# Kernel tuning notes

Measured on AMD Instinct MI355X. Metric: run time of the kernel, lower is better.

Reference implementation:

```python
import jax, jax.numpy as jnp
import numpy as np

N = [80000, 70000, 50000]   # entities per type (flattened over the ragged batch)
F = [64, 128, 48]           # feature width per entity type
D = 512                     # d_model
B = 64                      # number of episodes in the ragged batch
EPS_IN = 1e-4               # InputNorm eps
EPS_LN = 1e-5               # LayerNorm eps
CLIP = 5.0                  # InputNorm cliprange


def setup_inputs() -> dict:
    key = jax.random.key(0)
    ks = jax.random.split(key, 3 * 7 + 2)
    inp = {}
    for i, (n, f) in enumerate(zip(N, F)):
        base = 7 * i
        inp[f"ent{i}"] = jax.random.normal(ks[base], (n, f), dtype=jnp.float32)
        inp[f"mean{i}"] = 0.1 * jax.random.normal(ks[base + 1], (f,), dtype=jnp.float32)
        inp[f"var{i}"] = jax.random.uniform(ks[base + 2], (f,), minval=0.5, maxval=1.5, dtype=jnp.float32)
        inp[f"W{i}"] = jax.random.normal(ks[base + 3], (f, D), dtype=jnp.float32) / np.sqrt(f)
        inp[f"b{i}"] = jnp.zeros((D,), dtype=jnp.float32)
        inp[f"gamma{i}"] = jnp.ones((D,), dtype=jnp.float32)
        inp[f"beta{i}"] = jnp.zeros((D,), dtype=jnp.float32)
    total = sum(N)
    # index_map: permutation reassembling per-type blocks into ragged episode order
    inp["index_map"] = jax.random.permutation(ks[-2], total).astype(jnp.int64)
    inp["batch_index"] = jnp.sort(jax.random.randint(ks[-1], (total,), 0, B)).astype(jnp.int64)
    return inp


def _embed(x, mean, var, W, b, gamma, beta):
    # InputNorm: normalize with running stats, clip outliers
    h = jnp.clip((x - mean) * jax.lax.rsqrt(var + EPS_IN), -CLIP, CLIP)
    # Linear + ReLU
    h = jnp.maximum(h @ W + b, 0.0)
    # LayerNorm
    mu = h.mean(-1, keepdims=True)
    v = ((h - mu) ** 2).mean(-1, keepdims=True)
    return gamma * (h - mu) * jax.lax.rsqrt(v + EPS_LN) + beta


def reference(ent0, mean0, var0, W0, b0, gamma0, beta0,
              ent1, mean1, var1, W1, b1, gamma1, beta1,
              ent2, mean2, var2, W2, b2, gamma2, beta2,
              index_map, batch_index):
    embeds = [
        _embed(ent0, mean0, var0, W0, b0, gamma0, beta0),
        _embed(ent1, mean1, var1, W1, b1, gamma1, beta1),
        _embed(ent2, mean2, var2, W2, b2, gamma2, beta2),
    ]
    x = jnp.concatenate(embeds, axis=0)                      # [sum(N), D]
    entity_type = jnp.concatenate(
        [jnp.full((n, 1), float(i), dtype=jnp.float32) for i, n in enumerate(N)], axis=0
    )
    # ragged reorder: gather-based reassembly into episode-major order
    x = x[index_map]
    entity_types = entity_type[index_map]
    tbatch_index = batch_index[index_map]
    return x, tbatch_index, entity_types
```

## Files before the change

kernel.cpp:

```cpp
#include <hip/hip_runtime.h>

#define DMODEL 512
#define EPS_IN 1e-4f
#define EPS_LN 1e-5f
#define CLIPV  5.0f

typedef float f32x4 __attribute__((ext_vector_type(4)));
typedef short s16x8 __attribute__((ext_vector_type(8)));

__device__ __forceinline__ unsigned short f2bf(float f) {
    union { float f; unsigned u; } v; v.f = f;
    unsigned r = v.u + 0x7fffu + ((v.u >> 16) & 1u);
    return (unsigned short)(r >> 16);
}

struct TypeParams {
    const float* x;
    const float* ss;
    const unsigned short* Wt;
    const float* b; const float* gamma; const float* beta;
    int n;
    int offset;
    int nb;
};

__global__ __launch_bounds__(256) void setup_all(
    const int* __restrict__ index_map, const int* __restrict__ batch_index,
    int* __restrict__ inv, float* __restrict__ out_t, float* __restrict__ out_e,
    int total, int n0, int n01, int nbA,
    const float* __restrict__ W0, const float* __restrict__ W1, const float* __restrict__ W2,
    unsigned short* __restrict__ Wt0, unsigned short* __restrict__ Wt1, unsigned short* __restrict__ Wt2,
    const float* __restrict__ mean0, const float* __restrict__ var0,
    const float* __restrict__ mean1, const float* __restrict__ var1,
    const float* __restrict__ mean2, const float* __restrict__ var2,
    float* __restrict__ ss0, float* __restrict__ ss1, float* __restrict__ ss2)
{
    const int nbB = (DMODEL * 256) / 256;
    if (blockIdx.x < (unsigned)nbA) {
        const int j = blockIdx.x * 256 + threadIdx.x;
        if (j >= total) return;
        const int r = index_map[j];
        inv[r] = j;
        out_t[j] = (float)batch_index[r];
        out_e[j] = (r < n0) ? 0.0f : ((r < n01) ? 1.0f : 2.0f);
    } else if (blockIdx.x < (unsigned)(nbA + nbB)) {
        int idx = (blockIdx.x - nbA) * 256 + threadIdx.x;
        const float* W; unsigned short* Wt; int K, Kp;
        if (idx < DMODEL * 64)              { W = W0; Wt = Wt0; K = 64;  Kp = 64; }
        else if (idx < DMODEL * (64 + 128)) { idx -= DMODEL * 64;  W = W1; Wt = Wt1; K = 128; Kp = 128; }
        else                                { idx -= DMODEL * 192; W = W2; Wt = Wt2; K = 48;  Kp = 64; }
        const int nn = idx / Kp, k = idx - nn * Kp;
        const float w = (k < K) ? W[(size_t)k * DMODEL + nn] : 0.0f;
        Wt[idx] = f2bf(w);
    } else {
        const int c = threadIdx.x;
        if (c < 64)  { const float s = rsqrtf(var0[c] + EPS_IN); ss0[c] = s; ss0[64 + c]  = -mean0[c] * s; }
        if (c < 128) { const float s = rsqrtf(var1[c] + EPS_IN); ss1[c] = s; ss1[128 + c] = -mean1[c] * s; }
        if (c < 48)  { const float s = rsqrtf(var2[c] + EPS_IN); ss2[c] = s; ss2[48 + c]  = -mean2[c] * s; }
    }
}

template<int F, int KP>
__device__ __forceinline__ void embed_body(
    const TypeParams& p, int bid, const int* __restrict__ inv,
    float* __restrict__ out, char* lds)
{
    const int tid  = threadIdx.x;
    const int lane = tid & 63;
    const int wn   = tid >> 6;
    const int l15  = lane & 15;
    const int g    = lane >> 4;
    const int row0 = bid * 32;
    const int n    = p.n;
    constexpr int SEG = KP / 8;
    constexpr int NKS = KP / 32;

    float2* red = reinterpret_cast<float2*>(lds + NKS * 2048);

    if (tid < 32 * SEG) {
        const int r = tid & 31;
        const int s = tid >> 5;
        const int gr = row0 + r;
        const int c = s * 8;
        s16x8 pk;
#pragma unroll
        for (int jj = 0; jj < 8; ++jj) pk[jj] = 0;
        if (gr < n && c < F) {
            const float4 x0 = *(const float4*)(p.x + (size_t)gr * F + c);
            const float4 x1 = *(const float4*)(p.x + (size_t)gr * F + c + 4);
            const float4 sc0 = *(const float4*)(p.ss + c);
            const float4 sc1 = *(const float4*)(p.ss + c + 4);
            const float4 sh0 = *(const float4*)(p.ss + F + c);
            const float4 sh1 = *(const float4*)(p.ss + F + c + 4);
            float t[8];
            t[0] = fmaf(x0.x, sc0.x, sh0.x); t[1] = fmaf(x0.y, sc0.y, sh0.y);
            t[2] = fmaf(x0.z, sc0.z, sh0.z); t[3] = fmaf(x0.w, sc0.w, sh0.w);
            t[4] = fmaf(x1.x, sc1.x, sh1.x); t[5] = fmaf(x1.y, sc1.y, sh1.y);
            t[6] = fmaf(x1.z, sc1.z, sh1.z); t[7] = fmaf(x1.w, sc1.w, sh1.w);
#pragma unroll
            for (int jj = 0; jj < 8; ++jj)
                pk[jj] = (short)f2bf(fminf(fmaxf(t[jj], -CLIPV), CLIPV));
        }
        *reinterpret_cast<s16x8*>(lds + tid * 16) = pk;
    }
    __syncthreads();

    int orow[8];
#pragma unroll
    for (int m = 0; m < 2; ++m)
#pragma unroll
        for (int j = 0; j < 4; ++j) {
            const int rg = row0 + m * 16 + 4 * g + j;
            orow[m * 4 + j] = (rg < n) ? inv[p.offset + rg] : -1;
        }

    f32x4 acc[2][4];
#pragma unroll
    for (int m = 0; m < 2; ++m)
#pragma unroll
        for (int t = 0; t < 4; ++t) acc[m][t] = (f32x4)0.0f;

    const unsigned short* wtl = p.Wt + (size_t)(wn * 64 + l15) * KP + g * 8;

#pragma unroll
    for (int ks = 0; ks < NKS; ++ks) {
        const int ab = ((ks * 4 + g) * 32 + l15) * 16;
        const s16x8 a0 = *reinterpret_cast<const s16x8*>(lds + ab);
        const s16x8 a1 = *reinterpret_cast<const s16x8*>(lds + ab + 256);
#pragma unroll
        for (int t = 0; t < 4; ++t) {
            const s16x8 bf = *reinterpret_cast<const s16x8*>(wtl + (size_t)t * 16 * KP + ks * 32);
            acc[0][t] = __builtin_amdgcn_mfma_f32_16x16x32_bf16(a0, bf, acc[0][t], 0, 0, 0);
            acc[1][t] = __builtin_amdgcn_mfma_f32_16x16x32_bf16(a1, bf, acc[1][t], 0, 0, 0);
        }
    }

    float bv[4], gv[4], ev[4];
#pragma unroll
    for (int t = 0; t < 4; ++t) {
        const int col = wn * 64 + t * 16 + l15;
        bv[t] = p.b[col]; gv[t] = p.gamma[col]; ev[t] = p.beta[col];
    }

    {
        float ps[2][4] = {{0}}, pq[2][4] = {{0}};
#pragma unroll
        for (int m = 0; m < 2; ++m)
#pragma unroll
            for (int t = 0; t < 4; ++t)
#pragma unroll
                for (int j = 0; j < 4; ++j) {
                    const float v = fmaxf(acc[m][t][j] + bv[t], 0.0f);
                    ps[m][j] += v;
                    pq[m][j] = fmaf(v, v, pq[m][j]);
                }
#pragma unroll
        for (int off = 1; off < 16; off <<= 1)
#pragma unroll
            for (int m = 0; m < 2; ++m)
#pragma unroll
                for (int j = 0; j < 4; ++j) {
                    ps[m][j] += __shfl_xor(ps[m][j], off, 64);
                    pq[m][j] += __shfl_xor(pq[m][j], off, 64);
                }
        if (l15 == 0) {
#pragma unroll
            for (int m = 0; m < 2; ++m)
#pragma unroll
                for (int j = 0; j < 4; ++j) {
                    const int rl = m * 16 + 4 * g + j;
                    red[rl * 8 + wn] = make_float2(ps[m][j], pq[m][j]);
                }
        }
    }
    __syncthreads();

#pragma unroll
    for (int m = 0; m < 2; ++m)
#pragma unroll
        for (int j = 0; j < 4; ++j) {
            const int od = orow[m * 4 + j];
            if (od < 0) continue;
            const int rl = m * 16 + 4 * g + j;
            float s = 0.0f, q = 0.0f;
#pragma unroll
            for (int wq = 0; wq < 8; ++wq) { const float2 e = red[rl * 8 + wq]; s += e.x; q += e.y; }
            const float mu = s * (1.0f / DMODEL);
            const float vv = fmaxf(q * (1.0f / DMODEL) - mu * mu, 0.0f);
            const float sc = rsqrtf(vv + EPS_LN);
            float* op = out + (size_t)od * DMODEL + wn * 64 + l15;
#pragma unroll
            for (int t = 0; t < 4; ++t) {
                const float v = fmaxf(acc[m][t][j] + bv[t], 0.0f);
                op[t * 16] = fmaf(gv[t] * sc, v - mu, ev[t]);
            }
        }
}

__global__ __launch_bounds__(512, 4) void embed_all(
    TypeParams p0, TypeParams p1, TypeParams p2,
    const int* __restrict__ inv, float* __restrict__ out)
{
    extern __shared__ char lds[];
    const int bid = blockIdx.x;
    if (bid < p0.nb)                embed_body<64, 64>  (p0, bid, inv, out, lds);
    else if (bid < p0.nb + p1.nb)   embed_body<128, 128>(p1, bid - p0.nb, inv, out, lds);
    else                            embed_body<48, 64>  (p2, bid - p0.nb - p1.nb, inv, out, lds);
}

extern "C" void kernel_launch(void* const* d_in, const int* in_sizes, int n_in,
                              void* d_out, int out_size, void* d_ws, size_t ws_size,
                              hipStream_t stream)
{
    const int F0 = 64, F1 = 128, F2 = 48;
    const int n0 = in_sizes[0]  / F0;
    const int n1 = in_sizes[7]  / F1;
    const int n2 = in_sizes[14] / F2;
    const int total = n0 + n1 + n2;

    float* out   = (float*)d_out;
    float* out_t = out + (size_t)total * DMODEL;
    float* out_e = out_t + total;

    int* inv = (int*)d_ws;
    unsigned short* Wt0 = (unsigned short*)((char*)d_ws + (((size_t)total * 4 + 255) & ~(size_t)255));
    unsigned short* Wt1 = Wt0 + DMODEL * 64;
    unsigned short* Wt2 = Wt1 + DMODEL * 128;
    float* ss0 = (float*)(Wt2 + DMODEL * 64);
    float* ss1 = ss0 + 128;
    float* ss2 = ss1 + 256;

    const int* index_map   = (const int*)d_in[21];
    const int* batch_index = (const int*)d_in[22];

    const int nbA = (total + 255) / 256;
    const int nbB = (DMODEL * 256) / 256;
    setup_all<<<nbA + nbB + 1, 256, 0, stream>>>(
        index_map, batch_index, inv, out_t, out_e, total, n0, n0 + n1, nbA,
        (const float*)d_in[3], (const float*)d_in[10], (const float*)d_in[17],
        Wt0, Wt1, Wt2,
        (const float*)d_in[1],  (const float*)d_in[2],
        (const float*)d_in[8],  (const float*)d_in[9],
        (const float*)d_in[15], (const float*)d_in[16],
        ss0, ss1, ss2);

    TypeParams p0{(const float*)d_in[0],  ss0, Wt0,
                  (const float*)d_in[4],  (const float*)d_in[5],  (const float*)d_in[6],
                  n0, 0,       (n0 + 31) / 32};
    TypeParams p1{(const float*)d_in[7],  ss1, Wt1,
                  (const float*)d_in[11], (const float*)d_in[12], (const float*)d_in[13],
                  n1, n0,      (n1 + 31) / 32};
    TypeParams p2{(const float*)d_in[14], ss2, Wt2,
                  (const float*)d_in[18], (const float*)d_in[19], (const float*)d_in[20],
                  n2, n0 + n1, (n2 + 31) / 32};

    const int nb = p0.nb + p1.nb + p2.nb;
    const int lds_size = 4 * 2048 + 32 * 8 * sizeof(float2);
    embed_all<<<nb, 512, lds_size, stream>>>(p0, p1, p2, inv, out);
}
```

Measured before the change: 161.0 us.

## Swap MFMA operands so each lane owns a row for vectorized scatter stores

```diff
diff --git a/kernel.cpp b/kernel.cpp
--- a/kernel.cpp
+++ b/kernel.cpp
@@ -105,14 +105,12 @@
     }
     __syncthreads();
 
-    int orow[8];
-#pragma unroll
-    for (int m = 0; m < 2; ++m)
-#pragma unroll
-        for (int j = 0; j < 4; ++j) {
-            const int rg = row0 + m * 16 + 4 * g + j;
-            orow[m * 4 + j] = (rg < n) ? inv[p.offset + rg] : -1;
-        }
+    int orow[2];
+#pragma unroll
+    for (int m = 0; m < 2; ++m) {
+        const int rg = row0 + m * 16 + l15;
+        orow[m] = (rg < n) ? inv[p.offset + rg] : -1;
+    }
 
     f32x4 acc[2][4];
 #pragma unroll
@@ -129,75 +127,78 @@
         const s16x8 a1 = *reinterpret_cast<const s16x8*>(lds + ab + 256);
 #pragma unroll
         for (int t = 0; t < 4; ++t) {
-            const s16x8 bf = *reinterpret_cast<const s16x8*>(wtl + (size_t)t * 16 * KP + ks * 32);
-            acc[0][t] = __builtin_amdgcn_mfma_f32_16x16x32_bf16(a0, bf, acc[0][t], 0, 0, 0);
-            acc[1][t] = __builtin_amdgcn_mfma_f32_16x16x32_bf16(a1, bf, acc[1][t], 0, 0, 0);
-        }
-    }
-
-    float bv[4], gv[4], ev[4];
+            const s16x8 wf = *reinterpret_cast<const s16x8*>(wtl + (size_t)t * 16 * KP + ks * 32);
+            acc[0][t] = __builtin_amdgcn_mfma_f32_16x16x32_bf16(wf, a0, acc[0][t], 0, 0, 0);
+            acc[1][t] = __builtin_amdgcn_mfma_f32_16x16x32_bf16(wf, a1, acc[1][t], 0, 0, 0);
+        }
+    }
+
 #pragma unroll
     for (int t = 0; t < 4; ++t) {
-        const int col = wn * 64 + t * 16 + l15;
-        bv[t] = p.b[col]; gv[t] = p.gamma[col]; ev[t] = p.beta[col];
+        const float4 bb = *(const float4*)(p.b + wn * 64 + t * 16 + g * 4);
+#pragma unroll
+        for (int m = 0; m < 2; ++m) {
+            acc[m][t][0] = fmaxf(acc[m][t][0] + bb.x, 0.0f);
+            acc[m][t][1] = fmaxf(acc[m][t][1] + bb.y, 0.0f);
+            acc[m][t][2] = fmaxf(acc[m][t][2] + bb.z, 0.0f);
+            acc[m][t][3] = fmaxf(acc[m][t][3] + bb.w, 0.0f);
+        }
     }
 
     {
-        float ps[2][4] = {{0}}, pq[2][4] = {{0}};
+        float ps[2] = {0.0f, 0.0f}, pq[2] = {0.0f, 0.0f};
 #pragma unroll
         for (int m = 0; m < 2; ++m)
 #pragma unroll
             for (int t = 0; t < 4; ++t)
 #pragma unroll
                 for (int j = 0; j < 4; ++j) {
-                    const float v = fmaxf(acc[m][t][j] + bv[t], 0.0f);
-                    ps[m][j] += v;
-                    pq[m][j] = fmaf(v, v, pq[m][j]);
+                    const float v = acc[m][t][j];
+                    ps[m] += v;
+                    pq[m] = fmaf(v, v, pq[m]);
                 }
 #pragma unroll
-        for (int off = 1; off < 16; off <<= 1)
+        for (int m = 0; m < 2; ++m) {
+            ps[m] += __shfl_xor(ps[m], 16, 64);
+            pq[m] += __shfl_xor(pq[m], 16, 64);
+            ps[m] += __shfl_xor(ps[m], 32, 64);
+            pq[m] += __shfl_xor(pq[m], 32, 64);
+        }
+        if (g == 0) {
 #pragma unroll
             for (int m = 0; m < 2; ++m)
-#pragma unroll
-                for (int j = 0; j < 4; ++j) {
-                    ps[m][j] += __shfl_xor(ps[m][j], off, 64);
-                    pq[m][j] += __shfl_xor(pq[m][j], off, 64);
-                }
-        if (l15 == 0) {
-#pragma unroll
-            for (int m = 0; m < 2; ++m)
-#pragma unroll
-                for (int j = 0; j < 4; ++j) {
-                    const int rl = m * 16 + 4 * g + j;
-                    red[rl * 8 + wn] = make_float2(ps[m][j], pq[m][j]);
-                }
+                red[(m * 16 + l15) * 8 + wn] = make_float2(ps[m], pq[m]);
         }
     }
     __syncthreads();
 
 #pragma unroll
-    for (int m = 0; m < 2; ++m)
-#pragma unroll
-        for (int j = 0; j < 4; ++j) {
-            const int od = orow[m * 4 + j];
-            if (od < 0) continue;
-            const int rl = m * 16 + 4 * g + j;
-            float s = 0.0f, q = 0.0f;
-#pragma unroll
-            for (int wq = 0; wq < 8; ++wq) { const float2 e = red[rl * 8 + wq]; s += e.x; q += e.y; }
-            const float mu = s * (1.0f / DMODEL);
-            const float vv = fmaxf(q * (1.0f / DMODEL) - mu * mu, 0.0f);
-            const float sc = rsqrtf(vv + EPS_LN);
-            float* op = out + (size_t)od * DMODEL + wn * 64 + l15;
-#pragma unroll
-            for (int t = 0; t < 4; ++t) {
-                const float v = fmaxf(acc[m][t][j] + bv[t], 0.0f);
-                op[t * 16] = fmaf(gv[t] * sc, v - mu, ev[t]);
-            }
-        }
-}
-
-__global__ __launch_bounds__(512, 4) void embed_all(
+    for (int m = 0; m < 2; ++m) {
+        const int od = orow[m];
+        if (od < 0) continue;
+        const int rl = m * 16 + l15;
+        float s = 0.0f, q = 0.0f;
+#pragma unroll
+        for (int wq = 0; wq < 8; ++wq) { const float2 e = red[rl * 8 + wq]; s += e.x; q += e.y; }
+        const float mu = s * (1.0f / DMODEL);
+        const float vv = fmaxf(q * (1.0f / DMODEL) - mu * mu, 0.0f);
+        const float sc = rsqrtf(vv + EPS_LN);
+        float* op = out + (size_t)od * DMODEL + wn * 64 + g * 4;
+#pragma unroll
+        for (int t = 0; t < 4; ++t) {
+            const float4 gg = *(const float4*)(p.gamma + wn * 64 + t * 16 + g * 4);
+            const float4 ee = *(const float4*)(p.beta  + wn * 64 + t * 16 + g * 4);
+            float4 o;
+            o.x = fmaf(gg.x * sc, acc[m][t][0] - mu, ee.x);
+            o.y = fmaf(gg.y * sc, acc[m][t][1] - mu, ee.y);
+            o.z = fmaf(gg.z * sc, acc[m][t][2] - mu, ee.z);
+            o.w = fmaf(gg.w * sc, acc[m][t][3] - mu, ee.w);
+            *(float4*)(op + t * 16) = o;
+        }
+    }
+}
+
+__global__ __launch_bounds__(512, 6) void embed_all(
     TypeParams p0, TypeParams p1, TypeParams p2,
     const int* __restrict__ inv, float* __restrict__ out)
 {
```

Result: slower. 185.8 us (+15.4%).
